# Optimization experiments

Measured on AMD Instinct MI355X. Metric: run time of the kernel, lower is better.

Reference implementation:

```python
import jax, jax.numpy as jnp
import numpy as np

N = 8192
C = 128
K = 20          # neighbors per dilation branch
DILS = (1, 2)   # dilations
K_FULL = K * max(DILS)  # neighbors in the base knn graph
R = 4           # upsampling ratio
N_IDGCN = 2     # inception blocks
NEG_SLOPE_CONV = 0.2
NEG_SLOPE_MLP = 0.01  # torch LeakyReLU default in reconstructor


def knn_idx(pos, k):
    # brute-force knn on [N,3]; exclude self by taking k+1 and dropping col 0
    sq = jnp.sum(pos * pos, axis=-1)                       # [N]
    d = sq[:, None] + sq[None, :] - 2.0 * (pos @ pos.T)    # [N,N]
    _, idx = jax.lax.top_k(-d, k + 1)                      # nearest first
    return idx[:, 1:]                                      # [N,k]


def edge_conv(x, idx, W, b):
    # EdgeConv: max_j LeakyReLU(W @ [x_i, x_j - x_i] + b)
    xj = x[idx]                                            # [N,k,C] gather
    xi = jnp.broadcast_to(x[:, None, :], xj.shape)
    e = jnp.concatenate([xi, xj - xi], axis=-1)            # [N,k,2C]
    h = jax.nn.leaky_relu(e @ W + b, NEG_SLOPE_CONV)
    return jnp.max(h, axis=1)                              # [N,Cout]


def setup_inputs() -> dict:
    key = jax.random.key(0)
    ks = jax.random.split(key, 10)
    s_lift = 1.0 / np.sqrt(6.0)
    s_gcn = 1.0 / np.sqrt(2.0 * C)
    s_mlp = 1.0 / np.sqrt(C)
    n_gcn = N_IDGCN * len(DILS)
    return {
        "x": jax.random.normal(ks[0], (N, 3), dtype=jnp.float32),
        "W0": jax.random.normal(ks[1], (6, C), dtype=jnp.float32) * s_lift,
        "b0": jnp.zeros((C,), dtype=jnp.float32),
        "Wg": jax.random.normal(ks[2], (n_gcn, 2 * C, C), dtype=jnp.float32) * s_gcn,
        "bg": jnp.zeros((n_gcn, C), dtype=jnp.float32),
        "Wu": jax.random.normal(ks[3], (2 * C, R * C), dtype=jnp.float32) * s_gcn,
        "bu": jnp.zeros((R * C,), dtype=jnp.float32),
        "Wr1": jax.random.normal(ks[4], (C, C), dtype=jnp.float32) * s_mlp,
        "br1": jnp.zeros((C,), dtype=jnp.float32),
        "Wr2": jax.random.normal(ks[5], (C, 3), dtype=jnp.float32) * s_mlp,
        "br2": jnp.zeros((3,), dtype=jnp.float32),
    }


def reference(x, W0, b0, Wg, bg, Wu, bu, Wr1, br1, Wr2, br2):
    pos = x
    # knn graph on positions (k * max(dilations) neighbors)
    idx = knn_idx(pos, K_FULL)                             # [N, K_FULL]
    # lift 3 -> C with an EdgeConv on the first K neighbors
    h = edge_conv(pos, idx[:, :K], W0, b0)                 # [N, C]
    # Inception DenseGCN feature extractor: dilated EdgeConv branches + residual
    li = 0
    for _ in range(N_IDGCN):
        acc = jnp.zeros_like(h)
        for d in DILS:
            idx_d = idx[:, ::d][:, :K]                     # dilated neighbors
            acc = acc + edge_conv(h, idx_d, Wg[li], bg[li])
            li += 1
        h = h + acc / float(len(DILS))                     # residual
    # NodeShuffle upsampler: EdgeConv to r*C then shuffle nodes
    u = edge_conv(h, idx[:, :K], Wu, bu)                   # [N, r*C]
    u = u.reshape(N * R, C)                                # [N*r, C]
    # reconstructor MLP -> 3D coordinates
    q = jax.nn.leaky_relu(u @ Wr1 + br1, NEG_SLOPE_MLP)
    q = q @ Wr2 + br2                                      # [N*r, 3]
    return q
```

## Files before the change

### kernel.cpp

```cpp
#include <hip/hip_runtime.h>
#include <math.h>

#define N_PTS 8192
#define KFULL 40
#define KNB 20
#define QB 8
#define KBLK 512
#define NBK 1024
#define CAP 512

typedef unsigned short u16;
typedef unsigned int u32;
typedef unsigned long long u64;
typedef __attribute__((ext_vector_type(8))) short bf16x8;
typedef __attribute__((ext_vector_type(4))) float f32x4;

__device__ __forceinline__ u16 f2b(float v) {
  u32 u = __float_as_uint(v);
  return (u16)((u + 0x7FFFu + ((u >> 16) & 1u)) >> 16);
}
__device__ __forceinline__ u32 pk2(float a, float b) {
  return (u32)f2b(a) | ((u32)f2b(b) << 16);
}
__device__ __forceinline__ u32 dmap(float d) {
  u32 b = __float_as_uint(d);
  return b ^ ((u32)(((int)b) >> 31) | 0x80000000u);
}
__device__ __forceinline__ float inv_edge(int b) {
  if (b >= 1022) return 3.4e38f;
  const u32 m = (((u32)(b + 1)) << 22) - 1u;
  if (m < 0x80000000u) return 0.f;
  return __uint_as_float(m - 0x80000000u);
}
__device__ __forceinline__ void maxu4(const uint4 v, float m[8]) {
  m[0] = fmaxf(m[0], __uint_as_float(v.x << 16));
  m[1] = fmaxf(m[1], __uint_as_float(v.x & 0xFFFF0000u));
  m[2] = fmaxf(m[2], __uint_as_float(v.y << 16));
  m[3] = fmaxf(m[3], __uint_as_float(v.y & 0xFFFF0000u));
  m[4] = fmaxf(m[4], __uint_as_float(v.z << 16));
  m[5] = fmaxf(m[5], __uint_as_float(v.z & 0xFFFF0000u));
  m[6] = fmaxf(m[6], __uint_as_float(v.w << 16));
  m[7] = fmaxf(m[7], __uint_as_float(v.w & 0xFFFF0000u));
}
__device__ __forceinline__ void unp4(const uint4 v, float p[8]) {
  p[0] = __uint_as_float(v.x << 16);
  p[1] = __uint_as_float(v.x & 0xFFFF0000u);
  p[2] = __uint_as_float(v.y << 16);
  p[3] = __uint_as_float(v.y & 0xFFFF0000u);
  p[4] = __uint_as_float(v.z << 16);
  p[5] = __uint_as_float(v.z & 0xFFFF0000u);
  p[6] = __uint_as_float(v.w << 16);
  p[7] = __uint_as_float(v.w & 0xFFFF0000u);
}

typedef const __attribute__((address_space(1))) unsigned int* gas_p;
typedef __attribute__((address_space(3))) unsigned int* las_p;
__device__ __forceinline__ void gll16(const void* g, void* l) {
  __builtin_amdgcn_global_load_lds((gas_p)g, (las_p)l, 16, 0, 0);
}

__device__ __forceinline__ void scan_cut(const u32 (*hist)[NBK], int* s_cut,
                                         int t) {
  const int w = t >> 6, lane = t & 63;
  if (w < QB / 2) {
    const u32* H = hist[w];
    const int base = lane * (NBK / 64);
    u32 lsum = 0;
#pragma unroll
    for (int k = 0; k < NBK / 64; ++k) lsum += H[base + k];
    u32 inc = lsum;
#pragma unroll
    for (int off = 1; off < 64; off <<= 1) {
      const u32 u = __shfl_up(inc, off);
      if (lane >= off) inc += u;
    }
    const u32 excl = inc - lsum;
    const u32 TGT = KFULL + 1;
    const u32 exlo = excl & 0xFFFFu, inlo = inc & 0xFFFFu;
    if (exlo < TGT && inlo >= TGT) {
      u32 cum = exlo;
      for (int k = 0; k < NBK / 64; ++k) {
        cum += H[base + k] & 0xFFFFu;
        if (cum >= TGT) { s_cut[2 * w] = base + k; break; }
      }
    }
    const u32 exhi = excl >> 16, inhi = inc >> 16;
    if (exhi < TGT && inhi >= TGT) {
      u32 cum = exhi;
      for (int k = 0; k < NBK / 64; ++k) {
        cum += H[base + k] >> 16;
        if (cum >= TGT) { s_cut[2 * w + 1] = base + k; break; }
      }
    }
  }
}

__device__ __forceinline__ int scan_cut_wave(const u32* H, int lane) {
  const int base = lane * (NBK / 64);
  u32 lsum = 0;
#pragma unroll
  for (int k = 0; k < NBK / 64; ++k) lsum += H[base + k];
  u32 inc = lsum;
#pragma unroll
  for (int off = 1; off < 64; off <<= 1) {
    const u32 u = __shfl_up(inc, off);
    if (lane >= off) inc += u;
  }
  const u32 excl = inc - lsum;
  int cut = -1;
  if (excl < 41u && inc >= 41u) {
    u32 cum = excl;
    for (int k = 0; k < NBK / 64; ++k) {
      cum += H[base + k];
      if (cum >= 41u) { cut = base + k; break; }
    }
  }
  const u64 mask = __ballot(cut >= 0);
  if (mask == 0ull) return NBK - 1;
  const int src = __ffsll((long long)mask) - 1;
  return __shfl(cut, src);
}

__global__ __launch_bounds__(KBLK) void knn_kernel(const float4* __restrict__ pos4,
                                                   int* __restrict__ idx_out) {
  __shared__ __align__(16) u32 hmem[2 * QB * CAP];
  u32 (*hist)[NBK] = (u32(*)[NBK])hmem;
  u64 (*cand)[CAP] = (u64(*)[CAP])hmem;
  __shared__ float4 s_q[QB];
  __shared__ int s_cut[QB];
  __shared__ int s_cnt[QB];

  const int qb = blockIdx.x * QB, t = threadIdx.x;
  if (t < QB) {
    s_q[t] = pos4[qb + t];
    s_cnt[t] = 0;
  }
  for (int b = t; b < 4 * NBK; b += KBLK) hmem[b] = 0;
  __syncthreads();

  float qx[QB], qy[QB], qz[QB], qs[QB];
#pragma unroll
  for (int q = 0; q < QB; ++q) {
    const float4 v = s_q[q];
    qx[q] = -2.0f * v.x; qy[q] = -2.0f * v.y; qz[q] = -2.0f * v.z; qs[q] = v.w;
  }

  {
    const int j = t << 4;
    const float4 p = pos4[j];
#pragma unroll
    for (int q = 0; q < QB; ++q) {
      const float d = fmaf(qx[q], p.x, fmaf(qy[q], p.y, fmaf(qz[q], p.z, qs[q] + p.w)));
      atomicAdd(&hist[q >> 1][dmap(d) >> 22], 1u << ((q & 1) * 16));
    }
  }
  __syncthreads();
  scan_cut(hist, s_cut, t);
  __syncthreads();
  float r2a[QB];
#pragma unroll
  for (int q = 0; q < QB; ++q) r2a[q] = inv_edge(s_cut[q]);
  for (int b = t; b < 4 * NBK; b += KBLK) hmem[b] = 0;
  __syncthreads();

#pragma unroll 2
  for (int s = 0; s < 16; ++s) {
    const int j = t + (s << 9);
    const float4 p = pos4[j];
#pragma unroll
    for (int q = 0; q < QB; ++q) {
      const float d = fmaf(qx[q], p.x, fmaf(qy[q], p.y, fmaf(qz[q], p.z, qs[q] + p.w)));
      if (d <= r2a[q])
        atomicAdd(&hist[q >> 1][dmap(d) >> 22], 1u << ((q & 1) * 16));
    }
  }
  __syncthreads();
  scan_cut(hist, s_cut, t);
  __syncthreads();
  float r2b[QB];
#pragma unroll
  for (int q = 0; q < QB; ++q) r2b[q] = inv_edge(s_cut[q]);

#pragma unroll 2
  for (int s = 0; s < 16; ++s) {
    const int j = t + (s << 9);
    const float4 p = pos4[j];
#pragma unroll
    for (int q = 0; q < QB; ++q) {
      const float d = fmaf(qx[q], p.x, fmaf(qy[q], p.y, fmaf(qz[q], p.z, qs[q] + p.w)));
      if (d <= r2b[q]) {
        const int slot = atomicAdd(&s_cnt[q], 1);
        if (slot < CAP) cand[q][slot] = ((u64)dmap(d) << 13) | (u64)j;
      }
    }
  }
  __syncthreads();

  {
    const int w = t >> 6, lane = t & 63;
    int cnt = s_cnt[w];
    if (cnt > CAP) {
      const float4 qv = s_q[w];
      const float ax = -2.0f * qv.x, ay = -2.0f * qv.y, az = -2.0f * qv.z;
      const float aw = qv.w;
      const float R2w = inv_edge(s_cut[w]);
      u32* fbh = (u32*)cand[w];
      for (int b = lane; b < NBK; b += 64) fbh[b] = 0;
      for (int j = lane; j < N_PTS; j += 64) {
        const float4 p = pos4[j];
        const float d = fmaf(ax, p.x, fmaf(ay, p.y, fmaf(az, p.z, aw + p.w)));
        if (d <= R2w) atomicAdd(&fbh[dmap(d) >> 22], 1u);
      }
      const int cut2 = scan_cut_wave(fbh, lane);
      const float R2r = inv_edge(cut2);
      int base = 0;
      for (int j0 = 0; j0 < N_PTS; j0 += 64) {
        const int j = j0 + lane;
        const float4 p = pos4[j];
        const float d = fmaf(ax, p.x, fmaf(ay, p.y, fmaf(az, p.z, aw + p.w)));
        const bool pred = (d <= R2r);
        const u64 mask = __ballot(pred);
        if (pred) {
          const int off = __popcll(mask & ((1ull << lane) - 1ull));
          if (base + off < CAP)
            cand[w][base + off] = ((u64)dmap(d) << 13) | (u64)j;
        }
        base += (int)__popcll(mask);
      }
      cnt = base;
    }
    const int cmax = cnt < CAP ? cnt : CAP;
    for (int c0 = lane; c0 < cmax; c0 += 64) {
      const u64 my = cand[w][c0];
      int rank = 0;
      for (int c = 0; c < cmax; ++c) rank += (cand[w][c] < my) ? 1 : 0;
      if (rank >= 1 && rank <= KFULL)
        idx_out[(qb + w) * KFULL + (rank - 1)] = (int)(my & 0x1FFFull);
    }
  }
}

__device__ __forceinline__ void wcvt_body(const float* __restrict__ src,
                                          u16* __restrict__ dst, int ncols,
                                          int rows_per_tensor, int elems_per_tensor,
                                          int rg, int k) {
  const int li = rg / rows_per_tensor;
  const int r = rg % rows_per_tensor;
  const float* s = src + (size_t)li * elems_per_tensor;
  u16* d = dst + (size_t)li * elems_per_tensor;
  const int part = r / ncols, col = r % ncols;
  d[(size_t)r * 128 + k] = f2b(s[(size_t)(part * 128 + k) * ncols + col]);
}

__global__ __launch_bounds__(128) void prep_kernel(
    const float* __restrict__ x, const float* __restrict__ W0,
    const float* __restrict__ b0, const float* __restrict__ Wg,
    const float* __restrict__ Wu, const float* __restrict__ Wr1,
    float* __restrict__ Aout, u16* __restrict__ Pout, u16* __restrict__ Wgb,
    u16* __restrict__ Wub, u16* __restrict__ Wr1b, float4* __restrict__ pos4) {
  const int b = blockIdx.x, t = threadIdx.x;
  if (b < 8192) {
    const float px = x[b * 3 + 0], py = x[b * 3 + 1], pz = x[b * 3 + 2];
    const float a = b0[t] + px * W0[t] + py * W0[128 + t] + pz * W0[256 + t];
    const float p = px * W0[384 + t] + py * W0[512 + t] + pz * W0[640 + t];
    Aout[(size_t)b * 128 + t] = a;
    Pout[(size_t)b * 128 + t] = f2b(p);
  } else if (b < 9216) {
    wcvt_body(Wg, Wgb, 128, 256, 256 * 128, b - 8192, t);
  } else if (b < 10240) {
    wcvt_body(Wu, Wub, 512, 1024, 1024 * 128, b - 9216, t);
  } else if (b < 10368) {
    wcvt_body(Wr1, Wr1b, 128, 128, 128 * 128, b - 10240, t);
  } else {
    const int j = (b - 10368) * 128 + t;
    const float px = x[j * 3 + 0], py = x[j * 3 + 1], pz = x[j * 3 + 2];
    pos4[j] = make_float4(px, py, pz, px * px + py * py + pz * pz);
  }
}

__global__ __launch_bounds__(256) void gemm_mfma_kernel(
    const u16* __restrict__ Ain, const u16* __restrict__ Wt,
    const float* __restrict__ bias, int GA, int span_shift, int nAtot, int nPtot,
    float slope, int use_act, float* __restrict__ Aout, u16* __restrict__ Pout) {
  __shared__ __align__(16) u16 Al[128 * 128];
  __shared__ __align__(16) u16 Bl[64 * 128];
  const int bm = blockIdx.x * 128;
  const int bn = blockIdx.y * 64;
  const int tid = threadIdx.x;

#pragma unroll
  for (int it = 0; it < 8; ++it) {
    const int g = it * 256 + tid;
    const int row = g >> 4, cc = g & 15;
    const int sc = cc ^ (row & 7);
    gll16(Ain + (size_t)(bm + row) * 128 + sc * 8, &Al[g * 8]);
  }
#pragma unroll
  for (int it = 0; it < 4; ++it) {
    const int g = it * 256 + tid;
    const int row = g >> 4, cc = g & 15;
    const int sc = cc ^ (row & 7);
    gll16(Wt + (size_t)(bn + row) * 128 + sc * 8, &Bl[g * 8]);
  }
  __syncthreads();

  const int wv = tid >> 6, lane = tid & 63;
  const int wm = wv & 1, wn = wv >> 1;
  const int lr = lane & 15, lk = lane >> 4;

  bf16x8 a[4][4], b[2][4];
  f32x4 acc[4][2];
#pragma unroll
  for (int m = 0; m < 4; ++m)
#pragma unroll
    for (int n = 0; n < 2; ++n) acc[m][n] = (f32x4){0.f, 0.f, 0.f, 0.f};

#pragma unroll
  for (int m = 0; m < 4; ++m) {
    const int row = wm * 64 + m * 16 + lr;
#pragma unroll
    for (int ks = 0; ks < 4; ++ks) {
      const int c = ks * 4 + lk;
      a[m][ks] = *(const bf16x8*)&Al[row * 128 + (c ^ (row & 7)) * 8];
    }
  }
#pragma unroll
  for (int n = 0; n < 2; ++n) {
    const int col = wn * 32 + n * 16 + lr;
#pragma unroll
    for (int ks = 0; ks < 4; ++ks) {
      const int c = ks * 4 + lk;
      b[n][ks] = *(const bf16x8*)&Bl[col * 128 + (c ^ (col & 7)) * 8];
    }
  }

#pragma unroll
  for (int ks = 0; ks < 4; ++ks)
#pragma unroll
    for (int m = 0; m < 4; ++m)
#pragma unroll
      for (int n = 0; n < 2; ++n)
        acc[m][n] = __builtin_amdgcn_mfma_f32_16x16x32_bf16(a[m][ks], b[n][ks],
                                                            acc[m][n], 0, 0, 0);

  const int span = 1 << span_shift;
  const int GP = span - GA;
#pragma unroll
  for (int n = 0; n < 2; ++n) {
    const int col = bn + wn * 32 + n * 16 + lr;
    const int g = col >> span_shift;
    const int wi = col & (span - 1);
    const bool isA = wi < GA;
    const float bv = isA ? bias[g * GA + wi] : 0.f;
#pragma unroll
    for (int m = 0; m < 4; ++m) {
      const int row0 = bm + wm * 64 + m * 16 + lk * 4;
#pragma unroll
      for (int r = 0; r < 4; ++r) {
        float v = acc[m][n][r] + bv;
        if (isA) {
          if (use_act) v = v > 0.f ? v : v * slope;
          Aout[(size_t)(row0 + r) * nAtot + g * GA + wi] = v;
        } else {
          Pout[(size_t)(row0 + r) * nPtot + g * GP + (wi - GA)] = f2b(v);
        }
      }
    }
  }
}

__global__ __launch_bounds__(256) void gather_one_kernel(
    const float* __restrict__ A, const u16* __restrict__ P,
    const int* __restrict__ idx, int C, int dil, float* __restrict__ outf,
    u16* __restrict__ outb) {
  const int t = threadIdx.x;
  const int i = blockIdx.x * 16 + (t >> 4);
  const int c = blockIdx.y * 128 + (t & 15) * 8;
  float m[8];
#pragma unroll
  for (int k = 0; k < 8; ++k) m[k] = -INFINITY;
  const int ib = i * KFULL;
#pragma unroll
  for (int j = 0; j < KNB; ++j) {
    const int n = idx[ib + j * dil] & (N_PTS - 1);
    maxu4(*(const uint4*)&P[(size_t)n * C + c], m);
  }
  float pv[8];
  unp4(*(const uint4*)&P[(size_t)i * C + c], pv);
  const float4 a0 = *(const float4*)&A[(size_t)i * C + c];
  const float4 a1 = *(const float4*)&A[(size_t)i * C + c + 4];
  const float av[8] = {a0.x, a0.y, a0.z, a0.w, a1.x, a1.y, a1.z, a1.w};
  float v[8];
#pragma unroll
  for (int k = 0; k < 8; ++k) {
    const float x = av[k] - pv[k] + m[k];
    v[k] = x > 0.f ? x : 0.2f * x;
  }
  if (outf) {
    *(float4*)&outf[(size_t)i * C + c] = make_float4(v[0], v[1], v[2], v[3]);
    *(float4*)&outf[(size_t)i * C + c + 4] = make_float4(v[4], v[5], v[6], v[7]);
  }
  if (outb) {
    uint4 pb = {pk2(v[0], v[1]), pk2(v[2], v[3]), pk2(v[4], v[5]), pk2(v[6], v[7])};
    *(uint4*)&outb[(size_t)i * C + c] = pb;
  }
}

__global__ __launch_bounds__(256) void gather_pair_kernel(
    const float* __restrict__ Ap, const u16* __restrict__ Pp,
    const int* __restrict__ idx, float* __restrict__ h, u16* __restrict__ hb) {
  const int t = threadIdx.x;
  const int i = blockIdx.x * 16 + (t >> 4);
  const int c = (t & 15) * 8;
  float m1[8], m2[8];
#pragma unroll
  for (int k = 0; k < 8; ++k) { m1[k] = -INFINITY; m2[k] = -INFINITY; }
  const int ib = i * KFULL;
#pragma unroll
  for (int j = 0; j < KNB; ++j) {
    const int n1 = idx[ib + j] & (N_PTS - 1);
    maxu4(*(const uint4*)&Pp[(size_t)n1 * 256 + c], m1);
    const int n2 = idx[ib + 2 * j] & (N_PTS - 1);
    maxu4(*(const uint4*)&Pp[(size_t)n2 * 256 + 128 + c], m2);
  }
  float p0[8], p1[8];
  unp4(*(const uint4*)&Pp[(size_t)i * 256 + c], p0);
  unp4(*(const uint4*)&Pp[(size_t)i * 256 + 128 + c], p1);
  const float4 a00 = *(const float4*)&Ap[(size_t)i * 256 + c];
  const float4 a01 = *(const float4*)&Ap[(size_t)i * 256 + c + 4];
  const float4 a10 = *(const float4*)&Ap[(size_t)i * 256 + 128 + c];
  const float4 a11 = *(const float4*)&Ap[(size_t)i * 256 + 128 + c + 4];
  const float av0[8] = {a00.x, a00.y, a00.z, a00.w, a01.x, a01.y, a01.z, a01.w};
  const float av1[8] = {a10.x, a10.y, a10.z, a10.w, a11.x, a11.y, a11.z, a11.w};
  const float4 h0 = *(const float4*)&h[(size_t)i * 128 + c];
  const float4 h1 = *(const float4*)&h[(size_t)i * 128 + c + 4];
  const float hv[8] = {h0.x, h0.y, h0.z, h0.w, h1.x, h1.y, h1.z, h1.w};
  float v[8];
#pragma unroll
  for (int k = 0; k < 8; ++k) {
    float x1 = av0[k] - p0[k] + m1[k];
    x1 = x1 > 0.f ? x1 : 0.2f * x1;
    float x2 = av1[k] - p1[k] + m2[k];
    x2 = x2 > 0.f ? x2 : 0.2f * x2;
    v[k] = hv[k] + 0.5f * (x1 + x2);
  }
  *(float4*)&h[(size_t)i * 128 + c] = make_float4(v[0], v[1], v[2], v[3]);
  *(float4*)&h[(size_t)i * 128 + c + 4] = make_float4(v[4], v[5], v[6], v[7]);
  uint4 pb = {pk2(v[0], v[1]), pk2(v[2], v[3]), pk2(v[4], v[5]), pk2(v[6], v[7])};
  *(uint4*)&hb[(size_t)i * 128 + c] = pb;
}

__global__ __launch_bounds__(128) void recon2_kernel(const float* __restrict__ T,
                                                     const float* __restrict__ Wr2,
                                                     const float* __restrict__ br2,
                                                     float* __restrict__ out) {
  __shared__ float tile[32][129];
  __shared__ float w2[384];
  const int tid = threadIdx.x;
  const int r0 = blockIdx.x * 32;
  w2[tid] = Wr2[tid];
  w2[tid + 128] = Wr2[tid + 128];
  w2[tid + 256] = Wr2[tid + 256];
  for (int s = 0; s < 32; ++s) tile[s][tid] = T[(size_t)(r0 + s) * 128 + tid];
  __syncthreads();
  if (tid < 96) {
    const int r = tid / 3, n = tid % 3;
    float acc = br2[n];
#pragma unroll
    for (int k = 0; k < 128; ++k) acc = fmaf(tile[r][k], w2[k * 3 + n], acc);
    out[(size_t)(r0 + r) * 3 + n] = acc;
  }
}

extern "C" void kernel_launch(void* const* d_in, const int* in_sizes, int n_in,
                              void* d_out, int out_size, void* d_ws, size_t ws_size,
                              hipStream_t stream) {
  const float* x = (const float*)d_in[0];
  const float* W0 = (const float*)d_in[1];
  const float* b0 = (const float*)d_in[2];
  const float* Wg = (const float*)d_in[3];
  const float* bg = (const float*)d_in[4];
  const float* Wu = (const float*)d_in[5];
  const float* bu = (const float*)d_in[6];
  const float* Wr1 = (const float*)d_in[7];
  const float* br1 = (const float*)d_in[8];
  const float* Wr2 = (const float*)d_in[9];
  const float* br2 = (const float*)d_in[10];
  float* out = (float*)d_out;

  char* w = (char*)d_ws;
  int* idx = (int*)(w + 0);
  float4* pos4 = (float4*)(w + 1310720);
  float* h = (float*)(w + 1441792);
  u16* hb = (u16*)(w + 5636096);
  float* Apair = (float*)(w + 7733248);
  u16* Ppair = (u16*)(w + 16121856);
  u16* Wgb = (u16*)(w + 20316160);
  u16* Wub = (u16*)(w + 20578304);
  u16* Wr1b = (u16*)(w + 20840448);
  float* Abig = (float*)(w + 20873216);
  u16* Pbig = (u16*)(w + 37650432);
  u16* Ub = (u16*)Apair;
  float* T = Abig;

  prep_kernel<<<10432, 128, 0, stream>>>(x, W0, b0, Wg, Wu, Wr1, Abig, Pbig, Wgb,
                                         Wub, Wr1b, pos4);

  knn_kernel<<<N_PTS / QB, KBLK, 0, stream>>>(pos4, idx);

  gather_one_kernel<<<dim3(512, 1), 256, 0, stream>>>(Abig, Pbig, idx, 128, 1, h, hb);

  for (int blk = 0; blk < 2; ++blk) {
    const int li = blk * 2;
    gemm_mfma_kernel<<<dim3(64, 8), 256, 0, stream>>>(
        hb, Wgb + (size_t)li * 256 * 128, bg + li * 128, 128, 8, 256, 256, 0.f, 0,
        Apair, Ppair);
    gather_pair_kernel<<<512, 256, 0, stream>>>(Apair, Ppair, idx, h, hb);
  }

  gemm_mfma_kernel<<<dim3(64, 16), 256, 0, stream>>>(hb, Wub, bu, 512, 10, 512, 512,
                                                     0.f, 0, Abig, Pbig);
  gather_one_kernel<<<dim3(512, 4), 256, 0, stream>>>(Abig, Pbig, idx, 512, 1,
                                                      (float*)nullptr, Ub);

  gemm_mfma_kernel<<<dim3(256, 2), 256, 0, stream>>>(Ub, Wr1b, br1, 128, 7, 128, 128,
                                                     0.01f, 1, T, (u16*)nullptr);
  recon2_kernel<<<1024, 128, 0, stream>>>(T, Wr2, br2, out);
}
```

Measured before the change: 165.8 us.

## Split knn refinement histogram into two copies and store MLP hidden in bf16

The knn refinement pass now gives each half of the block its own shared-memory histogram copy, which should reduce LDS atomic contention. The scan merges the two copies when computing the cutoff. The reconstructor's first GEMM writes its hidden activations as bf16 instead of fp32, and recon2 reads them back as bf16, halving that intermediate's memory traffic. The cost is an extra histogram clear and merge in the scan, plus a small precision loss on the hidden layer.

New measurement: 170.4 us. 1.03x slower.

```diff
diff --git a/kernel.cpp b/kernel.cpp
--- a/kernel.cpp
+++ b/kernel.cpp
@@ -18,6 +18,9 @@
 __device__ __forceinline__ u16 f2b(float v) {
   u32 u = __float_as_uint(v);
   return (u16)((u + 0x7FFFu + ((u >> 16) & 1u)) >> 16);
+}
+__device__ __forceinline__ float b2f(u16 b) {
+  return __uint_as_float(((u32)b) << 16);
 }
 __device__ __forceinline__ u32 pk2(float a, float b) {
   return (u32)f2b(a) | ((u32)f2b(b) << 16);
@@ -59,15 +62,20 @@
   __builtin_amdgcn_global_load_lds((gas_p)g, (las_p)l, 16, 0, 0);
 }
 
-__device__ __forceinline__ void scan_cut(const u32 (*hist)[NBK], int* s_cut,
+__device__ __forceinline__ void scan_cut(const u32* hmem, int dual, int* s_cut,
                                          int t) {
   const int w = t >> 6, lane = t & 63;
   if (w < QB / 2) {
-    const u32* H = hist[w];
+    const u32* H = hmem + w * NBK;
+    const u32* H2 = H + 4 * NBK;
     const int base = lane * (NBK / 64);
     u32 lsum = 0;
 #pragma unroll
-    for (int k = 0; k < NBK / 64; ++k) lsum += H[base + k];
+    for (int k = 0; k < NBK / 64; ++k) {
+      u32 v = H[base + k];
+      if (dual) v += H2[base + k];
+      lsum += v;
+    }
     u32 inc = lsum;
 #pragma unroll
     for (int off = 1; off < 64; off <<= 1) {
@@ -80,7 +88,9 @@
     if (exlo < TGT && inlo >= TGT) {
       u32 cum = exlo;
       for (int k = 0; k < NBK / 64; ++k) {
-        cum += H[base + k] & 0xFFFFu;
+        u32 v = H[base + k];
+        if (dual) v += H2[base + k];
+        cum += v & 0xFFFFu;
         if (cum >= TGT) { s_cut[2 * w] = base + k; break; }
       }
     }
@@ -88,7 +98,9 @@
     if (exhi < TGT && inhi >= TGT) {
       u32 cum = exhi;
       for (int k = 0; k < NBK / 64; ++k) {
-        cum += H[base + k] >> 16;
+        u32 v = H[base + k];
+        if (dual) v += H2[base + k];
+        cum += v >> 16;
         if (cum >= TGT) { s_cut[2 * w + 1] = base + k; break; }
       }
     }
@@ -125,6 +137,7 @@
                                                    int* __restrict__ idx_out) {
   __shared__ __align__(16) u32 hmem[2 * QB * CAP];
   u32 (*hist)[NBK] = (u32(*)[NBK])hmem;
+  u32 (*hist2)[NBK] = (u32(*)[NBK])(hmem + 4 * NBK);
   u64 (*cand)[CAP] = (u64(*)[CAP])hmem;
   __shared__ float4 s_q[QB];
   __shared__ int s_cut[QB];
@@ -155,27 +168,30 @@
     }
   }
   __syncthreads();
-  scan_cut(hist, s_cut, t);
+  scan_cut(hmem, 0, s_cut, t);
   __syncthreads();
   float r2a[QB];
 #pragma unroll
   for (int q = 0; q < QB; ++q) r2a[q] = inv_edge(s_cut[q]);
-  for (int b = t; b < 4 * NBK; b += KBLK) hmem[b] = 0;
-  __syncthreads();
-
+  for (int b = t; b < 8 * NBK; b += KBLK) hmem[b] = 0;
+  __syncthreads();
+
+  {
+    u32 (*myh)[NBK] = (t < 256) ? hist : hist2;
 #pragma unroll 2
-  for (int s = 0; s < 16; ++s) {
-    const int j = t + (s << 9);
-    const float4 p = pos4[j];
-#pragma unroll
-    for (int q = 0; q < QB; ++q) {
-      const float d = fmaf(qx[q], p.x, fmaf(qy[q], p.y, fmaf(qz[q], p.z, qs[q] + p.w)));
-      if (d <= r2a[q])
-        atomicAdd(&hist[q >> 1][dmap(d) >> 22], 1u << ((q & 1) * 16));
-    }
-  }
-  __syncthreads();
-  scan_cut(hist, s_cut, t);
+    for (int s = 0; s < 16; ++s) {
+      const int j = t + (s << 9);
+      const float4 p = pos4[j];
+#pragma unroll
+      for (int q = 0; q < QB; ++q) {
+        const float d = fmaf(qx[q], p.x, fmaf(qy[q], p.y, fmaf(qz[q], p.z, qs[q] + p.w)));
+        if (d <= r2a[q])
+          atomicAdd(&myh[q >> 1][dmap(d) >> 22], 1u << ((q & 1) * 16));
+      }
+    }
+  }
+  __syncthreads();
+  scan_cut(hmem, 1, s_cut, t);
   __syncthreads();
   float r2b[QB];
 #pragma unroll
@@ -281,7 +297,8 @@
 __global__ __launch_bounds__(256) void gemm_mfma_kernel(
     const u16* __restrict__ Ain, const u16* __restrict__ Wt,
     const float* __restrict__ bias, int GA, int span_shift, int nAtot, int nPtot,
-    float slope, int use_act, float* __restrict__ Aout, u16* __restrict__ Pout) {
+    float slope, int use_act, float* __restrict__ Aout,
+    u16* __restrict__ Aout16, u16* __restrict__ Pout) {
   __shared__ __align__(16) u16 Al[128 * 128];
   __shared__ __align__(16) u16 Bl[64 * 128];
   const int bm = blockIdx.x * 128;
@@ -360,7 +377,10 @@
         float v = acc[m][n][r] + bv;
         if (isA) {
           if (use_act) v = v > 0.f ? v : v * slope;
-          Aout[(size_t)(row0 + r) * nAtot + g * GA + wi] = v;
+          if (Aout16)
+            Aout16[(size_t)(row0 + r) * nAtot + g * GA + wi] = f2b(v);
+          else
+            Aout[(size_t)(row0 + r) * nAtot + g * GA + wi] = v;
         } else {
           Pout[(size_t)(row0 + r) * nPtot + g * GP + (wi - GA)] = f2b(v);
         }
@@ -450,7 +470,7 @@
   *(uint4*)&hb[(size_t)i * 128 + c] = pb;
 }
 
-__global__ __launch_bounds__(128) void recon2_kernel(const float* __restrict__ T,
+__global__ __launch_bounds__(128) void recon2_kernel(const u16* __restrict__ Tb,
                                                      const float* __restrict__ Wr2,
                                                      const float* __restrict__ br2,
                                                      float* __restrict__ out) {
@@ -461,7 +481,8 @@
   w2[tid] = Wr2[tid];
   w2[tid + 128] = Wr2[tid + 128];
   w2[tid + 256] = Wr2[tid + 256];
-  for (int s = 0; s < 32; ++s) tile[s][tid] = T[(size_t)(r0 + s) * 128 + tid];
+  for (int s = 0; s < 32; ++s)
+    tile[s][tid] = b2f(Tb[(size_t)(r0 + s) * 128 + tid]);
   __syncthreads();
   if (tid < 96) {
     const int r = tid / 3, n = tid % 3;
@@ -501,7 +522,7 @@
   float* Abig = (float*)(w + 20873216);
   u16* Pbig = (u16*)(w + 37650432);
   u16* Ub = (u16*)Apair;
-  float* T = Abig;
+  u16* Tb = (u16*)Abig;
 
   prep_kernel<<<10432, 128, 0, stream>>>(x, W0, b0, Wg, Wu, Wr1, Abig, Pbig, Wgb,
                                          Wub, Wr1b, pos4);
@@ -514,16 +535,18 @@
     const int li = blk * 2;
     gemm_mfma_kernel<<<dim3(64, 8), 256, 0, stream>>>(
         hb, Wgb + (size_t)li * 256 * 128, bg + li * 128, 128, 8, 256, 256, 0.f, 0,
-        Apair, Ppair);
+        Apair, (u16*)nullptr, Ppair);
     gather_pair_kernel<<<512, 256, 0, stream>>>(Apair, Ppair, idx, h, hb);
   }
 
   gemm_mfma_kernel<<<dim3(64, 16), 256, 0, stream>>>(hb, Wub, bu, 512, 10, 512, 512,
-                                                     0.f, 0, Abig, Pbig);
+                                                     0.f, 0, Abig, (u16*)nullptr,
+                                                     Pbig);
   gather_one_kernel<<<dim3(512, 4), 256, 0, stream>>>(Abig, Pbig, idx, 512, 1,
                                                       (float*)nullptr, Ub);
 
   gemm_mfma_kernel<<<dim3(256, 2), 256, 0, stream>>>(Ub, Wr1b, br1, 128, 7, 128, 128,
-                                                     0.01f, 1, T, (u16*)nullptr);
-  recon2_kernel<<<1024, 128, 0, stream>>>(T, Wr2, br2, out);
-}
+                                                     0.01f, 1, (float*)nullptr, Tb,
+                                                     (u16*)nullptr);
+  recon2_kernel<<<1024, 128, 0, stream>>>(Tb, Wr2, br2, out);
+}
```
